# Performance work log

Hardware: AMD Instinct MI355X
Metric: run time of the kernel (lower is better)

The kernel has to match this reference:

```python
import jax, jax.numpy as jnp
import numpy as np
from jax import lax

D = 512      # d_model
H = 8        # millions_moe_n_heads
DK = 128     # millions_moe_d_keys
HALF = DK // 2
E = 256      # moe_n_experts (per sub-key set); total experts = E*E = 65536
K = 16       # moe_top_k
N, T = 2, 512


def setup_inputs() -> dict:
    key = jax.random.key(0)
    ks = jax.random.split(key, 6)
    bound = 1.0 / np.sqrt(D)      # nn.Linear default init range
    kb = 1.0 / np.sqrt(HALF)      # get_uniform_keys bound
    queries = jax.random.normal(ks[0], (N, T, D), jnp.float32)
    Wq = jax.random.uniform(ks[1], (H * DK, D), jnp.float32, -bound, bound)
    bq = jax.random.uniform(ks[2], (H * DK,), jnp.float32, -bound, bound)
    keys = jax.random.uniform(ks[3], (H, 2, E, HALF), jnp.float32, -kb, kb)
    w_down_embed = jax.random.normal(ks[4], (E * E, D), jnp.float32) * (D ** -0.5)
    w_up_embed = jax.random.normal(ks[5], (E * E, D), jnp.float32) * (D ** -0.5)
    return {"queries": queries, "Wq": Wq, "bq": bq, "keys": keys,
            "w_down_embed": w_down_embed, "w_up_embed": w_up_embed}


def reference(queries, Wq, bq, keys, w_down_embed, w_up_embed):
    n, t, d = queries.shape
    NT = n * t
    # query projection: (NT, H, DK)
    qh = (queries.reshape(NT, d) @ Wq.T + bq).reshape(NT, H, DK)
    q1, q2 = qh[..., :HALF], qh[..., HALF:]
    # sub-key scores per head, vectorized over heads: (NT, H, E)
    s1 = jnp.einsum('nhc,hec->nhe', q1, keys[:, 0])
    s2 = jnp.einsum('nhc,hec->nhe', q2, keys[:, 1])
    s1, i1 = lax.top_k(s1, K)   # (NT, H, K)
    s2, i2 = lax.top_k(s2, K)
    # cartesian product of the two top-k sets: (NT, H, K*K)
    all_scores = (s1[..., :, None] + s2[..., None, :]).reshape(NT, H, K * K)
    all_indices = (i1[..., :, None] * E + i2[..., None, :]).reshape(NT, H, K * K)
    scores, best = lax.top_k(all_scores, K)                        # (NT, H, K)
    indices = jnp.take_along_axis(all_indices, best, axis=-1)      # (NT, H, K)
    scores = scores.reshape(NT * H, K)
    indices = indices.reshape(NT * H, K)
    # dynamic expert gathers
    w_down = w_down_embed[indices]   # (NT*H, K, D)
    w_up = w_up_embed[indices]       # (NT*H, K, D)
    # faithful to torch einsum ellipsis broadcasting in the source:
    # queries (N,T,D) x w_down (NT*H,K,D) -> (N,T,NT*H,K)
    qk = jnp.einsum('ntd,mkd->ntmk', queries, w_down)
    qk = jax.nn.relu(qk)
    values = qk * jax.nn.softmax(scores, axis=-1)   # broadcast (NT*H,K)
    out = jnp.einsum('ntmk,mkd->ntd', values, w_up)  # sum over all NT*H and K
    return out.reshape(n, t, d)
```

## Files before the change

kernel.cpp:

```cpp
#include <hip/hip_runtime.h>
#include <stdint.h>

#define NTOK 1024
#define DIM  512
#define NH   8
#define DKH  128
#define HALFD 64
#define EXP  256
#define EE   65536
#define HDK  1024

typedef short bf16x8 __attribute__((ext_vector_type(8)));
typedef float f32x4  __attribute__((ext_vector_type(4)));

__device__ __forceinline__ unsigned short f2bf(float f) {
    unsigned u = __float_as_uint(f);
    u += 0x7fff + ((u >> 16) & 1);
    return (unsigned short)(u >> 16);
}
__device__ __forceinline__ float bf2f(unsigned short h) {
    return __uint_as_float((unsigned)h << 16);
}

__device__ __forceinline__ unsigned long long mkkey(float x, int idx) {
    unsigned u = __float_as_uint(x);
    unsigned mu = u ^ ((unsigned)((int)u >> 31) | 0x80000000u);
    return ((unsigned long long)mu << 32) | (unsigned)(255 - idx);
}
__device__ __forceinline__ float keyval(unsigned long long k) {
    unsigned mu = (unsigned)(k >> 32);
    unsigned u = (mu & 0x80000000u) ? (mu ^ 0x80000000u) : ~mu;
    return __uint_as_float(u);
}

__device__ __forceinline__ unsigned long long sel16(unsigned long long k) {
    unsigned long long T = 0;
#pragma unroll
    for (int b = 63; b >= 32; --b) {
        unsigned long long C = T | (1ULL << b);
        if (__popcll(__ballot(k >= C)) >= 16) T = C;
    }
#pragma unroll
    for (int b = 7; b >= 0; --b) {
        unsigned long long C = T | (1ULL << b);
        if (__popcll(__ballot(k >= C)) >= 16) T = C;
    }
    return T;
}

__device__ __forceinline__ void gload16(const unsigned short* g, unsigned short* l) {
    __builtin_amdgcn_global_load_lds(
        (const __attribute__((address_space(1))) void*)g,
        (__attribute__((address_space(3))) void*)l, 16, 0, 0);
}

__device__ __constant__ unsigned char qtab[64] = {
    0, 1, 2, 3, 4, 5, 6, 7, 8, 9, 10, 11, 12, 13, 14, 15,
    16, 17, 18, 19, 20, 21, 22, 23,
    32, 33, 34, 35, 36,
    48, 49, 50, 51,
    64, 65, 66,
    80, 81, 96, 97, 112, 113,
    128, 144, 160, 176, 192, 208, 224, 240,
    0, 0, 0, 0, 0, 0, 0, 0, 0, 0, 0, 0, 0, 0};

__global__ void cvt_bf16(const float* __restrict__ src,
                         unsigned short* __restrict__ dst, int n8) {
    int i = blockIdx.x * blockDim.x + threadIdx.x;
    if (i >= n8) return;
    const float4* s4 = (const float4*)src;
    float4 a = s4[2 * i], b = s4[2 * i + 1];
    union { unsigned short u[8]; uint4 v; } r;
    r.u[0] = f2bf(a.x); r.u[1] = f2bf(a.y); r.u[2] = f2bf(a.z); r.u[3] = f2bf(a.w);
    r.u[4] = f2bf(b.x); r.u[5] = f2bf(b.y); r.u[6] = f2bf(b.z); r.u[7] = f2bf(b.w);
    ((uint4*)dst)[i] = r.v;
}

template <int MODE>
__global__ void cvt_pack(const float* __restrict__ src,
                         unsigned short* __restrict__ dst) {
    int i = blockIdx.x * blockDim.x + threadIdx.x;
    if (i >= 131072) return;
    int r = i >> 7, c4 = i & 127;
    float4 a = ((const float4*)src)[i];
    union { unsigned short u[4]; uint2 v; } rh, rl;
    float x[4] = {a.x, a.y, a.z, a.w};
#pragma unroll
    for (int j = 0; j < 4; j++) {
        unsigned short h = f2bf(x[j]);
        rh.u[j] = h;
        rl.u[j] = f2bf(x[j] - bf2f(h));
    }
    uint2* A2 = (uint2*)dst;
    A2[r * 384 + c4] = rh.v;
    A2[r * 384 + 128 + c4] = (MODE == 0) ? rh.v : rl.v;
    A2[r * 384 + 256 + c4] = (MODE == 0) ? rl.v : rh.v;
}

__global__ void transpose_wu(const float* __restrict__ wu,
                             unsigned short* __restrict__ wuT, int e0base) {
    __shared__ float tile[64][65];
    int d0 = blockIdx.x * 64;
    int e0 = blockIdx.y * 64;
    int tid = threadIdx.x;

    int lr = tid >> 4;
    int lc = tid & 15;
#pragma unroll
    for (int p = 0; p < 4; p++) {
        int e = lr + 16 * p;
        float4 v = *(const float4*)&wu[(size_t)(e0base + e0 + e) * DIM + d0 + lc * 4];
        tile[e][lc * 4 + 0] = v.x;
        tile[e][lc * 4 + 1] = v.y;
        tile[e][lc * 4 + 2] = v.z;
        tile[e][lc * 4 + 3] = v.w;
    }
    __syncthreads();

    int dr = tid >> 3;
    int ec = tid & 7;
#pragma unroll
    for (int p = 0; p < 2; p++) {
        int d = dr + 32 * p;
        union { unsigned short u[8]; uint4 v; } r;
#pragma unroll
        for (int k = 0; k < 8; k++) r.u[k] = f2bf(tile[ec * 8 + k][d]);
        *(uint4*)&wuT[(size_t)(d0 + d) * 32768 + e0 + ec * 8] = r.v;
    }
}

template <int EPI>
__global__ __launch_bounds__(256, 4) void gemm_bt(
    const unsigned short* __restrict__ A, int lda,
    const unsigned short* __restrict__ B, int ldb,
    int kIters,
    float* __restrict__ outF, unsigned short* __restrict__ outB, int ldc,
    const float* __restrict__ scale, size_t sliceStride) {
    __shared__ __align__(16) unsigned short As[128 * 64];
    __shared__ __align__(16) unsigned short Bs[128 * 64];

    int nwg = gridDim.x * gridDim.y * gridDim.z;
    int flat = blockIdx.x + gridDim.x * (blockIdx.y + gridDim.y * blockIdx.z);
    int swz;
    if ((nwg & 7) == 0) {
        int chunk = nwg >> 3;
        swz = (flat & 7) * chunk + (flat >> 3);
    } else {
        swz = flat;
    }
    int bx = swz % gridDim.x;
    int tmp = swz / gridDim.x;
    int by = tmp % gridDim.y;
    int bz = tmp / gridDim.y;

    int tid = threadIdx.x;
    int lane = tid & 63, wave = tid >> 6;
    int wm = (wave >> 1) * 64, wn = (wave & 1) * 64;
    int row0 = bx * 128, col0 = by * 128;
    size_t k00 = (size_t)bz * kIters * 64;

    int rr = tid >> 3;
    int ss = tid & 7;
    int kb = ss ^ (rr & 7);
    const unsigned short* Ab = A + (size_t)(row0 + rr) * lda + k00 + kb * 8;
    const unsigned short* Bb = B + (size_t)(col0 + rr) * ldb + k00 + kb * 8;
    unsigned short* Asw = As + (size_t)tid * 8;
    unsigned short* Bsw = Bs + (size_t)tid * 8;

    f32x4 acc[4][4];
#pragma unroll
    for (int i = 0; i < 4; i++)
#pragma unroll
        for (int j = 0; j < 4; j++) acc[i][j] = 0.f;

    for (int kt = 0; kt < kIters; ++kt) {
        __syncthreads();
#pragma unroll
        for (int i = 0; i < 4; i++)
            gload16(Ab + (size_t)(32 * i) * lda + kt * 64, Asw + i * 2048);
#pragma unroll
        for (int i = 0; i < 4; i++)
            gload16(Bb + (size_t)(32 * i) * ldb + kt * 64, Bsw + i * 2048);
        __syncthreads();
#pragma unroll
        for (int ks = 0; ks < 2; ks++) {
            bf16x8 af[4], bfr[4];
#pragma unroll
            for (int i = 0; i < 4; i++) {
                int m = wm + i * 16 + (lane & 15);
                int kq = ks * 4 + (lane >> 4);
                af[i]  = *(const bf16x8*)(As + m * 64 + ((kq ^ (m & 7)) * 8));
                int n = wn + i * 16 + (lane & 15);
                bfr[i] = *(const bf16x8*)(Bs + n * 64 + ((kq ^ (n & 7)) * 8));
            }
#pragma unroll
            for (int i = 0; i < 4; i++)
#pragma unroll
                for (int j = 0; j < 4; j++)
                    acc[i][j] = __builtin_amdgcn_mfma_f32_16x16x32_bf16(
                        af[i], bfr[j], acc[i][j], 0, 0, 0);
        }
    }

#pragma unroll
    for (int i = 0; i < 4; i++) {
        int rbase = row0 + wm + i * 16 + (lane >> 4) * 4;
#pragma unroll
        for (int j = 0; j < 4; j++) {
            int c = col0 + wn + j * 16 + (lane & 15);
#pragma unroll
            for (int r2 = 0; r2 < 4; r2++) {
                float v = acc[i][j][r2];
                int row = rbase + r2;
                if (EPI == 0) {
                    outF[(size_t)row * ldc + c] = v;
                } else if (EPI == 1) {
                    outB[(size_t)row * ldc + c] = f2bf(fmaxf(v, 0.f) * scale[c]);
                } else {
                    outB[(size_t)bz * sliceStride + (size_t)row * ldc + c] =
                        f2bf(v);
                }
            }
        }
    }
}

__global__ void reduce_part(const unsigned short* __restrict__ part,
                            float* __restrict__ out) {
    int i = blockIdx.x * blockDim.x + threadIdx.x;
    const uint4* p4 = (const uint4*)part;
    float s[8];
#pragma unroll
    for (int j = 0; j < 8; j++) s[j] = 0.f;
    for (int sl = 0; sl < 64; sl++) {
        uint4 t = p4[(size_t)sl * 65536 + i];
        unsigned uu[4] = {t.x, t.y, t.z, t.w};
#pragma unroll
        for (int j = 0; j < 4; j++) {
            s[2 * j]     += bf2f((unsigned short)(uu[j] & 0xffff));
            s[2 * j + 1] += bf2f((unsigned short)(uu[j] >> 16));
        }
    }
    float4* o4 = (float4*)out;
    o4[2 * i]     = make_float4(s[0], s[1], s[2], s[3]);
    o4[2 * i + 1] = make_float4(s[4], s[5], s[6], s[7]);
}

__global__ __launch_bounds__(256) void score_all(
    const float* __restrict__ qh, const float* __restrict__ bq,
    const float* __restrict__ keys, float* __restrict__ S) {
    int t0 = blockIdx.x * 16;
    int h  = blockIdx.y;
    int half = blockIdx.z;
    int tid = threadIdx.x;

    __shared__ __align__(16) float qs[16 * 64];

    const float4* krow =
        (const float4*)(keys + (size_t)((h * 2 + half) * EXP + tid) * HALFD);
    float4 kreg[16];
#pragma unroll
    for (int c = 0; c < 16; c++) kreg[c] = krow[c];

    {
        int t = tid >> 4, c4 = tid & 15;
        const float4* qsrc =
            (const float4*)(qh + (size_t)(t0 + t) * HDK + h * DKH + half * HALFD);
        const float4* bsrc = (const float4*)(bq + h * DKH + half * HALFD);
        float4 qv = qsrc[c4], bv = bsrc[c4];
        ((float4*)qs)[t * 16 + c4] =
            make_float4(qv.x + bv.x, qv.y + bv.y, qv.z + bv.z, qv.w + bv.w);
    }
    __syncthreads();

    float acc[16];
#pragma unroll
    for (int t = 0; t < 16; t++) acc[t] = 0.f;
#pragma unroll
    for (int c = 0; c < 16; c++) {
        float4 kv = kreg[c];
#pragma unroll
        for (int t = 0; t < 16; t++) {
            float4 qv = ((const float4*)qs)[t * 16 + c];
            acc[t] += kv.x * qv.x + kv.y * qv.y + kv.z * qv.z + kv.w * qv.w;
        }
    }

#pragma unroll
    for (int t = 0; t < 16; t++)
        S[(size_t)(((t0 + t) * NH + h) * 2 + half) * EXP + tid] = acc[t];
}

__global__ __launch_bounds__(256) void topk_sel(
    const float* __restrict__ S, float* __restrict__ w) {
    int nt = blockIdx.x, h = blockIdx.y;
    int tid = threadIdx.x;
    int lane = tid & 63, wv = tid >> 6;

    __shared__ __align__(16) unsigned long long c1k[64], c2k[64];
    __shared__ float t1v[16], t2v[16];
    __shared__ int   t1i[16], t2i[16];
    __shared__ __align__(16) unsigned long long ck[64];
    __shared__ float selv[16];
    __shared__ int   seli[16];

    float v1 = S[(size_t)((nt * NH + h) * 2 + 0) * EXP + tid];
    float v2 = S[(size_t)((nt * NH + h) * 2 + 1) * EXP + tid];
    unsigned long long k1 = mkkey(v1, tid);
    unsigned long long k2 = mkkey(v2, tid);

    {
        unsigned long long T1 = sel16(k1);
        unsigned long long m1 = __ballot(k1 >= T1);
        if (k1 >= T1)
            c1k[wv * 16 + __popcll(m1 & ((1ULL << lane) - 1))] = k1;
        unsigned long long T2 = sel16(k2);
        unsigned long long m2 = __ballot(k2 >= T2);
        if (k2 >= T2)
            c2k[wv * 16 + __popcll(m2 & ((1ULL << lane) - 1))] = k2;
    }
    __syncthreads();

    if (wv < 2) {
        const unsigned long long* ak = wv ? c2k : c1k;
        unsigned long long mk = ak[lane];
        int r = 0;
#pragma unroll 4
        for (int j = 0; j < 64; j += 2) {
            ulonglong2 p = *(const ulonglong2*)&ak[j];
            r += (p.x > mk);
            r += (p.y > mk);
        }
        if (r < 16) {
            float v = keyval(mk);
            int e = 255 - (int)(mk & 0xff);
            if (wv == 0) { t1v[r] = v; t1i[r] = e; }
            else         { t2v[r] = v; t2i[r] = e; }
        }
    }
    __syncthreads();

    if (wv == 0) {
        int qq = (int)qtab[lane];
        bool act = lane < 50;
        float cval = t1v[qq >> 4] + t2v[qq & 15];
        unsigned long long k = act ? mkkey(cval, qq) : 0ULL;
        ck[lane] = k;
        asm volatile("s_waitcnt lgkmcnt(0)" ::: "memory");
        int r = 0;
#pragma unroll 5
        for (int j = 0; j < 50; j += 2) {
            ulonglong2 p = *(const ulonglong2*)&ck[j];
            r += (p.x > k);
            r += (p.y > k);
        }
        if (act && r < 16) {
            selv[r] = cval;
            seli[r] = t1i[qq >> 4] * EXP + t2i[qq & 15];
        }
        asm volatile("s_waitcnt lgkmcnt(0)" ::: "memory");
        if (lane < 16) {
            float val = selv[lane];
            float mx = selv[0];
#pragma unroll
            for (int j = 1; j < 16; j++) mx = fmaxf(mx, selv[j]);
            float sm = 0.f;
#pragma unroll
            for (int j = 0; j < 16; j++) sm += __expf(selv[j] - mx);
            atomicAdd(&w[seli[lane]], __expf(val - mx) / sm);
        }
    }
}

extern "C" void kernel_launch(void* const* d_in, const int* in_sizes, int n_in,
                              void* d_out, int out_size, void* d_ws, size_t ws_size,
                              hipStream_t stream) {
    const float* queries = (const float*)d_in[0];
    const float* Wq      = (const float*)d_in[1];
    const float* bq      = (const float*)d_in[2];
    const float* keys    = (const float*)d_in[3];
    const float* wd      = (const float*)d_in[4];
    const float* wu      = (const float*)d_in[5];
    float* out = (float*)d_out;

    uint8_t* ws = (uint8_t*)d_ws;
    const size_t MB = 1048576;
    unsigned short* Qcat  = (unsigned short*)(ws);
    float*          w     = (float*)(ws + 3 * MB);
    unsigned short* Wdh   = (unsigned short*)(ws + 4 * MB);
    unsigned short* WuTh  = (unsigned short*)(ws + 36 * MB);
    unsigned short* Cb    = (unsigned short*)(ws + 68 * MB);
    unsigned short* Ppart = (unsigned short*)(ws + 132 * MB);
    unsigned short* Wqcat = (unsigned short*)(ws + 132 * MB);
    float*          qh    = (float*)(ws + 135 * MB);
    float*          S     = (float*)(ws + 139 * MB);

    hipMemsetAsync(w, 0, EE * sizeof(float), stream);

    cvt_pack<0><<<512, 256, 0, stream>>>(queries, Qcat);
    cvt_pack<1><<<512, 256, 0, stream>>>(Wq, Wqcat);

    gemm_bt<0><<<dim3(8, 8, 1), 256, 0, stream>>>(
        Qcat, 1536, Wqcat, 1536, 24, qh, nullptr, HDK, nullptr, 0);

    score_all<<<dim3(64, NH, 2), 256, 0, stream>>>(qh, bq, keys, S);
    topk_sel<<<dim3(NTOK, NH), 256, 0, stream>>>(S, w);

    for (int sp = 0; sp < 2; sp++) {
        cvt_bf16<<<8192, 256, 0, stream>>>(wd + (size_t)sp * 16777216, Wdh, 2097152);
        gemm_bt<1><<<dim3(8, 256, 1), 256, 0, stream>>>(
            Qcat, 1536, Wdh, DIM, 8, nullptr, Cb, 32768, w + (size_t)sp * 32768, 0);
        transpose_wu<<<dim3(8, 512), 256, 0, stream>>>(wu, WuTh, sp * 32768);
        gemm_bt<4><<<dim3(8, 4, 32), 256, 0, stream>>>(
            Cb, 32768, WuTh, 32768, 16, nullptr,
            Ppart + (size_t)sp * 32 * 524288, DIM, nullptr, 524288);
    }
    reduce_part<<<256, 256, 0, stream>>>(Ppart, out);
}
```

Before: 524.7 us.

## Add 256x256-tile MFMA GEMM with 4-stage LDS pipeline for expert GEMMs

```diff
diff --git a/kernel.cpp b/kernel.cpp
--- a/kernel.cpp
+++ b/kernel.cpp
@@ -218,6 +218,143 @@
                     outB[(size_t)row * ldc + c] = f2bf(fmaxf(v, 0.f) * scale[c]);
                 } else {
                     outB[(size_t)bz * sliceStride + (size_t)row * ldc + c] =
+                        f2bf(v);
+                }
+            }
+        }
+    }
+}
+
+template <int EPI>
+__global__ __launch_bounds__(512, 2) void gemm256(
+    const unsigned short* __restrict__ A, int lda,
+    const unsigned short* __restrict__ B, int ldb,
+    int kIters,
+    unsigned short* __restrict__ outB, int ldc,
+    const float* __restrict__ scale, size_t sliceStride) {
+    __shared__ __align__(16) unsigned short As[4][256 * 32];
+    __shared__ __align__(16) unsigned short Bs[4][256 * 32];
+
+    int nwg = gridDim.x * gridDim.y * gridDim.z;
+    int flat = blockIdx.x + gridDim.x * (blockIdx.y + gridDim.y * blockIdx.z);
+    int chunk = nwg >> 3;
+    int swz = (flat & 7) * chunk + (flat >> 3);
+    int bx = swz % gridDim.x;
+    int tmp = swz / gridDim.x;
+    int by = tmp % gridDim.y;
+    int bz = tmp / gridDim.y;
+
+    int tid = threadIdx.x;
+    int lane = tid & 63;
+    int wave = tid >> 6;
+    int wm = (wave >> 2) * 128;
+    int wn = (wave & 3) * 64;
+    int row0 = bx * 256, col0 = by * 256;
+    size_t k00 = (size_t)bz * kIters * 32;
+
+    int rr = tid >> 2;
+    int ss = tid & 3;
+    int kb = ss ^ ((rr >> 1) & 3);
+    const unsigned short* Ab = A + (size_t)(row0 + rr) * lda + k00 + kb * 8;
+    const unsigned short* Bb = B + (size_t)(col0 + rr) * ldb + k00 + kb * 8;
+
+    auto stageA = [&](int kt_) {
+        int q_ = kt_ & 3;
+        gload16(Ab + (size_t)kt_ * 32, &As[q_][tid * 8]);
+        gload16(Ab + (size_t)128 * lda + (size_t)kt_ * 32, &As[q_][4096 + tid * 8]);
+    };
+    auto stageB = [&](int kt_) {
+        int q_ = kt_ & 3;
+        gload16(Bb + (size_t)kt_ * 32, &Bs[q_][tid * 8]);
+        gload16(Bb + (size_t)128 * ldb + (size_t)kt_ * 32, &Bs[q_][4096 + tid * 8]);
+    };
+
+    f32x4 acc[8][4];
+#pragma unroll
+    for (int f = 0; f < 8; f++)
+#pragma unroll
+        for (int c = 0; c < 4; c++) acc[f][c] = 0.f;
+
+    stageA(0); stageB(0);
+    stageA(1); stageB(1);
+    stageA(2); stageB(2);
+    asm volatile("s_waitcnt vmcnt(8)" ::: "memory");
+    __builtin_amdgcn_s_barrier();
+    asm volatile("" ::: "memory");
+
+    int kqs = lane >> 4;
+    for (int kt = 0; kt < kIters; ++kt) {
+        int q = kt & 3;
+        bool st = (kt + 3) < kIters;
+        const unsigned short* Aq = &As[q][0];
+        const unsigned short* Bq = &Bs[q][0];
+
+        bf16x8 bfr[4], af[4];
+#pragma unroll
+        for (int c = 0; c < 4; c++) {
+            int n = wn + c * 16 + (lane & 15);
+            bfr[c] = *(const bf16x8*)&Bq[n * 32 + ((kqs ^ ((n >> 1) & 3)) * 8)];
+        }
+#pragma unroll
+        for (int f = 0; f < 4; f++) {
+            int m = wm + f * 16 + (lane & 15);
+            af[f] = *(const bf16x8*)&Aq[m * 32 + ((kqs ^ ((m >> 1) & 3)) * 8)];
+        }
+        if (st) stageA(kt + 3);
+        asm volatile("" ::: "memory");
+        __builtin_amdgcn_s_barrier();
+        asm volatile("" ::: "memory");
+        __builtin_amdgcn_s_setprio(1);
+#pragma unroll
+        for (int f = 0; f < 4; f++)
+#pragma unroll
+            for (int c = 0; c < 4; c++)
+                acc[f][c] = __builtin_amdgcn_mfma_f32_16x16x32_bf16(
+                    af[f], bfr[c], acc[f][c], 0, 0, 0);
+        __builtin_amdgcn_s_setprio(0);
+        asm volatile("" ::: "memory");
+        __builtin_amdgcn_s_barrier();
+        asm volatile("" ::: "memory");
+
+        bf16x8 af2[4];
+#pragma unroll
+        for (int f = 0; f < 4; f++) {
+            int m = wm + 64 + f * 16 + (lane & 15);
+            af2[f] = *(const bf16x8*)&Aq[m * 32 + ((kqs ^ ((m >> 1) & 3)) * 8)];
+        }
+        if (st) stageB(kt + 3);
+        if (st)                        asm volatile("s_waitcnt vmcnt(8)" ::: "memory");
+        else if (kt == kIters - 3)     asm volatile("s_waitcnt vmcnt(4)" ::: "memory");
+        else if (kt == kIters - 2)     asm volatile("s_waitcnt vmcnt(0)" ::: "memory");
+        __builtin_amdgcn_s_barrier();
+        asm volatile("" ::: "memory");
+        __builtin_amdgcn_s_setprio(1);
+#pragma unroll
+        for (int f = 0; f < 4; f++)
+#pragma unroll
+            for (int c = 0; c < 4; c++)
+                acc[4 + f][c] = __builtin_amdgcn_mfma_f32_16x16x32_bf16(
+                    af2[f], bfr[c], acc[4 + f][c], 0, 0, 0);
+        __builtin_amdgcn_s_setprio(0);
+        asm volatile("" ::: "memory");
+        __builtin_amdgcn_s_barrier();
+        asm volatile("" ::: "memory");
+    }
+
+#pragma unroll
+    for (int f = 0; f < 8; f++) {
+        int rbase = row0 + wm + f * 16 + (lane >> 4) * 4;
+#pragma unroll
+        for (int c = 0; c < 4; c++) {
+            int cc = col0 + wn + c * 16 + (lane & 15);
+#pragma unroll
+            for (int r2 = 0; r2 < 4; r2++) {
+                float v = acc[f][c][r2];
+                int row = rbase + r2;
+                if (EPI == 1) {
+                    outB[(size_t)row * ldc + cc] = f2bf(fmaxf(v, 0.f) * scale[cc]);
+                } else {
+                    outB[(size_t)bz * sliceStride + (size_t)row * ldc + cc] =
                         f2bf(v);
                 }
             }
@@ -408,11 +545,11 @@
 
     for (int sp = 0; sp < 2; sp++) {
         cvt_bf16<<<8192, 256, 0, stream>>>(wd + (size_t)sp * 16777216, Wdh, 2097152);
-        gemm_bt<1><<<dim3(8, 256, 1), 256, 0, stream>>>(
-            Qcat, 1536, Wdh, DIM, 8, nullptr, Cb, 32768, w + (size_t)sp * 32768, 0);
+        gemm256<1><<<dim3(4, 128, 1), 512, 0, stream>>>(
+            Qcat, 1536, Wdh, DIM, 16, Cb, 32768, w + (size_t)sp * 32768, 0);
         transpose_wu<<<dim3(8, 512), 256, 0, stream>>>(wu, WuTh, sp * 32768);
-        gemm_bt<4><<<dim3(8, 4, 32), 256, 0, stream>>>(
-            Cb, 32768, WuTh, 32768, 16, nullptr,
+        gemm256<4><<<dim3(4, 2, 32), 512, 0, stream>>>(
+            Cb, 32768, WuTh, 32768, 32,
             Ppart + (size_t)sp * 32 * 524288, DIM, nullptr, 524288);
     }
     reduce_part<<<256, 256, 0, stream>>>(Ppart, out);
```

Measured after the change: 547.2 us. 4.3% more time.
